# Optimization experiments

Hardware: AMD Instinct MI355X
Metric: run time of the kernel (lower is better)

Reference implementation:

```python
import jax, jax.numpy as jnp
import numpy as np

B, C, D, T, N_SUBJ = 64, 1024, 1024, 1024, 32


def setup_inputs() -> dict:
    key = jax.random.key(0)
    k1, k2, k3 = jax.random.split(key, 3)
    x = jax.random.normal(k1, (B, C, T), dtype=jnp.float32)
    subjects = jax.random.randint(k2, (B,), 0, N_SUBJ, dtype=jnp.int64)
    # weights: normal_() then scaled by 1/sqrt(in_channels), as in __init__
    weights = jax.random.normal(k3, (N_SUBJ, C, D), dtype=jnp.float32) / np.sqrt(C).astype(np.float32)
    return {"x": x, "subjects": subjects, "weights": weights}


def reference(x, subjects, weights):
    # gather per-sample projection matrices: (B, C, D)
    w = weights[subjects]
    # out[b, d, t] = sum_c x[b, c, t] * w[b, c, d]
    return jnp.einsum('bct,bcd->bdt', x, w)
```

## Files before the change

kernel.cpp:

```cpp
#include <hip/hip_runtime.h>
#include <hip/hip_bf16.h>

typedef __attribute__((ext_vector_type(8))) short bf16x8;
typedef __attribute__((ext_vector_type(4))) float f32x4;
typedef __attribute__((ext_vector_type(4))) unsigned u32x4;

#define CDIM 1024
#define DDIM 1024
#define TDIM 1024
#define BK 32

__global__ __launch_bounds__(256, 2)
void subject_gemm(const float* __restrict__ x, const int* __restrict__ subj,
                  const float* __restrict__ w, float* __restrict__ out)
{
    __shared__ short Wt[128 * 64];
    __shared__ short Xt[128 * 64];

    const int bid = blockIdx.x;
    const int b = bid >> 6;
    const int r = bid & 63;
    const int dtile = (r >> 3) << 7;
    const int ttile = (r & 7) << 7;

    const int s = subj[b];
    const float* __restrict__ wB = w + (size_t)s * (CDIM * DDIM);
    const float* __restrict__ xB = x + (size_t)b * (CDIM * TDIM);

    const int tid = threadIdx.x;
    const int lane = tid & 63;
    const int wave = tid >> 6;

    const int sd = tid & 127;
    const int sc = (tid >> 7) << 4;
    const float* wp = wB + dtile + sd;
    const float* xp = xB + ttile + sd;
    short* wlds = Wt + sd * 64;
    short* xlds = Xt + sd * 64;
    const int swz = sd & 7;

    const int wr = (wave >> 1) << 6;
    const int wc = (wave & 1) << 6;
    const int fr = lane & 15;
    const int fg = lane >> 4;
    const int r7 = fr & 7;
    const int offH = (fg ^ r7) << 3;
    const int offL = ((fg + 4) ^ r7) << 3;

    f32x4 acc[4][4] = {};

    for (int k0 = 0; k0 < CDIM; k0 += BK) {
        float vw[16], vx[16];
        #pragma unroll
        for (int j = 0; j < 16; ++j) {
            const int c = k0 + sc + j;
            vw[j] = wp[c << 10];
            vx[j] = xp[c << 10];
        }
        u32x4 hwv[2], lwv[2], hxv[2], lxv[2];
        #pragma unroll
        for (int p = 0; p < 8; ++p) {
            {
                const float f0 = vw[2 * p], f1 = vw[2 * p + 1];
                const unsigned u0 = __float_as_uint(f0), u1 = __float_as_uint(f1);
                hwv[p >> 2][p & 3] = (u0 >> 16) | (u1 & 0xFFFF0000u);
                const float l0 = f0 - __uint_as_float(u0 & 0xFFFF0000u);
                const float l1 = f1 - __uint_as_float(u1 & 0xFFFF0000u);
                lwv[p >> 2][p & 3] = (__float_as_uint(l0) >> 16) | (__float_as_uint(l1) & 0xFFFF0000u);
            }
            {
                const float f0 = vx[2 * p], f1 = vx[2 * p + 1];
                const unsigned u0 = __float_as_uint(f0), u1 = __float_as_uint(f1);
                hxv[p >> 2][p & 3] = (u0 >> 16) | (u1 & 0xFFFF0000u);
                const float l0 = f0 - __uint_as_float(u0 & 0xFFFF0000u);
                const float l1 = f1 - __uint_as_float(u1 & 0xFFFF0000u);
                lxv[p >> 2][p & 3] = (__float_as_uint(l0) >> 16) | (__float_as_uint(l1) & 0xFFFF0000u);
            }
        }

        __syncthreads();
        #pragma unroll
        for (int g2 = 0; g2 < 2; ++g2) {
            const int g = (sc >> 3) + g2;
            *(u32x4*)(wlds + (((g    ) ^ swz) << 3)) = hwv[g2];
            *(u32x4*)(wlds + (((g + 4) ^ swz) << 3)) = lwv[g2];
            *(u32x4*)(xlds + (((g    ) ^ swz) << 3)) = hxv[g2];
            *(u32x4*)(xlds + (((g + 4) ^ swz) << 3)) = lxv[g2];
        }
        __syncthreads();

        bf16x8 ah[4], al[4], bh[4], bl[4];
        #pragma unroll
        for (int m = 0; m < 4; ++m) {
            const short* wrow = Wt + (wr + m * 16 + fr) * 64;
            ah[m] = *(const bf16x8*)(wrow + offH);
            al[m] = *(const bf16x8*)(wrow + offL);
            const short* xrow = Xt + (wc + m * 16 + fr) * 64;
            bh[m] = *(const bf16x8*)(xrow + offH);
            bl[m] = *(const bf16x8*)(xrow + offL);
        }
        #pragma unroll
        for (int m = 0; m < 4; ++m) {
            #pragma unroll
            for (int n = 0; n < 4; ++n) {
                acc[m][n] = __builtin_amdgcn_mfma_f32_16x16x32_bf16(ah[m], bh[n], acc[m][n], 0, 0, 0);
                acc[m][n] = __builtin_amdgcn_mfma_f32_16x16x32_bf16(ah[m], bl[n], acc[m][n], 0, 0, 0);
                acc[m][n] = __builtin_amdgcn_mfma_f32_16x16x32_bf16(al[m], bh[n], acc[m][n], 0, 0, 0);
            }
        }
    }

    float* __restrict__ oB = out + (size_t)b * (DDIM * TDIM)
                           + (size_t)(dtile + wr) * TDIM + (ttile + wc);
    #pragma unroll
    for (int m = 0; m < 4; ++m) {
        #pragma unroll
        for (int n = 0; n < 4; ++n) {
            #pragma unroll
            for (int q = 0; q < 4; ++q) {
                const int d = m * 16 + (fg << 2) + q;
                const int t = n * 16 + fr;
                oB[d * TDIM + t] = acc[m][n][q];
            }
        }
    }
}

extern "C" void kernel_launch(void* const* d_in, const int* in_sizes, int n_in,
                              void* d_out, int out_size, void* d_ws, size_t ws_size,
                              hipStream_t stream) {
    const float* x = (const float*)d_in[0];
    const int* subjects = (const int*)d_in[1];
    const float* w = (const float*)d_in[2];
    float* out = (float*)d_out;
    subject_gemm<<<dim3(64 * 8 * 8), dim3(256), 0, stream>>>(x, subjects, w, out);
}
```

Before: 464.0 us.

## Vectorize global loads, use hardware bf16 pack, XCD-aware block mapping, occupancy 3

Global loads change from scalar per-thread to float4 per thread, with half the threads loading W and half loading X. The truncating hi/lo bf16 split is replaced by the v_cvt_pk_bf16_f32 rounding instruction. Block IDs are remapped so each XCD handles a contiguous set of batch samples, which should improve L2 reuse of the shared subject weights. Launch bounds rise to 3 blocks per CU and A fragments are loaded per m to reduce register pressure. The rounding split changes numerics slightly, and the tighter register budget risks spills.

```diff
diff --git a/kernel.cpp b/kernel.cpp
--- a/kernel.cpp
+++ b/kernel.cpp
@@ -10,7 +10,13 @@
 #define TDIM 1024
 #define BK 32
 
-__global__ __launch_bounds__(256, 2)
+__device__ __forceinline__ unsigned cvt_pk_bf16(float a, float b) {
+    unsigned r;
+    asm("v_cvt_pk_bf16_f32 %0, %1, %2" : "=v"(r) : "v"(a), "v"(b));
+    return r;
+}
+
+__global__ __launch_bounds__(256, 3)
 void subject_gemm(const float* __restrict__ x, const int* __restrict__ subj,
                   const float* __restrict__ w, float* __restrict__ out)
 {
@@ -18,8 +24,10 @@
     __shared__ short Xt[128 * 64];
 
     const int bid = blockIdx.x;
-    const int b = bid >> 6;
-    const int r = bid & 63;
+    const int xcd = bid & 7;
+    const int slot = bid >> 3;
+    const int b = (xcd << 3) | (slot >> 6);
+    const int r = slot & 63;
     const int dtile = (r >> 3) << 7;
     const int ttile = (r & 7) << 7;
 
@@ -31,13 +39,13 @@
     const int lane = tid & 63;
     const int wave = tid >> 6;
 
-    const int sd = tid & 127;
-    const int sc = (tid >> 7) << 4;
-    const float* wp = wB + dtile + sd;
-    const float* xp = xB + ttile + sd;
-    short* wlds = Wt + sd * 64;
-    short* xlds = Xt + sd * 64;
-    const int swz = sd & 7;
+    const int ht = tid & 127;
+    const int tq = ht & 31;
+    const int cg = ht >> 5;
+    const int col0 = tq << 2;
+    const bool isW = (tid < 128);
+    const float* sp = (isW ? wB + dtile : xB + ttile) + col0;
+    short* slds = (isW ? Wt : Xt);
 
     const int wr = (wave >> 1) << 6;
     const int wc = (wave & 1) << 6;
@@ -50,62 +58,56 @@
     f32x4 acc[4][4] = {};
 
     for (int k0 = 0; k0 < CDIM; k0 += BK) {
-        float vw[16], vx[16];
+        float4 v4[8];
         #pragma unroll
-        for (int j = 0; j < 16; ++j) {
-            const int c = k0 + sc + j;
-            vw[j] = wp[c << 10];
-            vx[j] = xp[c << 10];
+        for (int j = 0; j < 8; ++j) {
+            const int c = k0 + (cg << 3) + j;
+            v4[j] = *(const float4*)(sp + ((size_t)c << 10));
         }
-        u32x4 hwv[2], lwv[2], hxv[2], lxv[2];
+
+        u32x4 hg[4], lg[4];
         #pragma unroll
-        for (int p = 0; p < 8; ++p) {
-            {
-                const float f0 = vw[2 * p], f1 = vw[2 * p + 1];
-                const unsigned u0 = __float_as_uint(f0), u1 = __float_as_uint(f1);
-                hwv[p >> 2][p & 3] = (u0 >> 16) | (u1 & 0xFFFF0000u);
-                const float l0 = f0 - __uint_as_float(u0 & 0xFFFF0000u);
-                const float l1 = f1 - __uint_as_float(u1 & 0xFFFF0000u);
-                lwv[p >> 2][p & 3] = (__float_as_uint(l0) >> 16) | (__float_as_uint(l1) & 0xFFFF0000u);
-            }
-            {
-                const float f0 = vx[2 * p], f1 = vx[2 * p + 1];
-                const unsigned u0 = __float_as_uint(f0), u1 = __float_as_uint(f1);
-                hxv[p >> 2][p & 3] = (u0 >> 16) | (u1 & 0xFFFF0000u);
-                const float l0 = f0 - __uint_as_float(u0 & 0xFFFF0000u);
-                const float l1 = f1 - __uint_as_float(u1 & 0xFFFF0000u);
-                lxv[p >> 2][p & 3] = (__float_as_uint(l0) >> 16) | (__float_as_uint(l1) & 0xFFFF0000u);
+        for (int rr = 0; rr < 4; ++rr) {
+            #pragma unroll
+            for (int p = 0; p < 4; ++p) {
+                const float f0 = v4[2 * p][rr];
+                const float f1 = v4[2 * p + 1][rr];
+                const unsigned h = cvt_pk_bf16(f0, f1);
+                const float l0 = f0 - __uint_as_float(h << 16);
+                const float l1 = f1 - __uint_as_float(h & 0xFFFF0000u);
+                hg[rr][p] = h;
+                lg[rr][p] = cvt_pk_bf16(l0, l1);
             }
         }
 
         __syncthreads();
         #pragma unroll
-        for (int g2 = 0; g2 < 2; ++g2) {
-            const int g = (sc >> 3) + g2;
-            *(u32x4*)(wlds + (((g    ) ^ swz) << 3)) = hwv[g2];
-            *(u32x4*)(wlds + (((g + 4) ^ swz) << 3)) = lwv[g2];
-            *(u32x4*)(xlds + (((g    ) ^ swz) << 3)) = hxv[g2];
-            *(u32x4*)(xlds + (((g + 4) ^ swz) << 3)) = lxv[g2];
+        for (int rr = 0; rr < 4; ++rr) {
+            const int row = col0 + rr;
+            short* sl = slds + row * 64;
+            const int swz = row & 7;
+            *(u32x4*)(sl + ((cg ^ swz) << 3)) = hg[rr];
+            *(u32x4*)(sl + (((cg + 4) ^ swz) << 3)) = lg[rr];
         }
         __syncthreads();
 
-        bf16x8 ah[4], al[4], bh[4], bl[4];
+        bf16x8 bh[4], bl[4];
+        #pragma unroll
+        for (int n = 0; n < 4; ++n) {
+            const short* xrow = Xt + (wc + n * 16 + fr) * 64;
+            bh[n] = *(const bf16x8*)(xrow + offH);
+            bl[n] = *(const bf16x8*)(xrow + offL);
+        }
         #pragma unroll
         for (int m = 0; m < 4; ++m) {
             const short* wrow = Wt + (wr + m * 16 + fr) * 64;
-            ah[m] = *(const bf16x8*)(wrow + offH);
-            al[m] = *(const bf16x8*)(wrow + offL);
-            const short* xrow = Xt + (wc + m * 16 + fr) * 64;
-            bh[m] = *(const bf16x8*)(xrow + offH);
-            bl[m] = *(const bf16x8*)(xrow + offL);
-        }
-        #pragma unroll
-        for (int m = 0; m < 4; ++m) {
+            const bf16x8 ah = *(const bf16x8*)(wrow + offH);
+            const bf16x8 al = *(const bf16x8*)(wrow + offL);
             #pragma unroll
             for (int n = 0; n < 4; ++n) {
-                acc[m][n] = __builtin_amdgcn_mfma_f32_16x16x32_bf16(ah[m], bh[n], acc[m][n], 0, 0, 0);
-                acc[m][n] = __builtin_amdgcn_mfma_f32_16x16x32_bf16(ah[m], bl[n], acc[m][n], 0, 0, 0);
-                acc[m][n] = __builtin_amdgcn_mfma_f32_16x16x32_bf16(al[m], bh[n], acc[m][n], 0, 0, 0);
+                acc[m][n] = __builtin_amdgcn_mfma_f32_16x16x32_bf16(ah, bh[n], acc[m][n], 0, 0, 0);
+                acc[m][n] = __builtin_amdgcn_mfma_f32_16x16x32_bf16(ah, bl[n], acc[m][n], 0, 0, 0);
+                acc[m][n] = __builtin_amdgcn_mfma_f32_16x16x32_bf16(al, bh[n], acc[m][n], 0, 0, 0);
             }
         }
     }
```

New measurement: 529.3 us. 14.1% more time.
